# Kernel tuning notes

Measured on AMD Instinct MI355X. Metric: run time of the kernel, lower is better.

The kernel has to match this reference:

```python
import jax, jax.numpy as jnp
import numpy as np

N_HEAD, D_MODEL, D_K, D_V, POS_DIM = 8, 512, 64, 64, 2
TEMPERATURE = 8.0
LN_EPS = 1e-6


def setup_inputs() -> dict:
    key = jax.random.key(0)
    ks = jax.random.split(key, 16)
    B, S = 4, 1024
    s = 0.02
    return {
        "q": jax.random.normal(ks[0], (B, S, D_MODEL), jnp.float32),
        "k": jax.random.normal(ks[1], (B, S, D_MODEL), jnp.float32),
        "v": jax.random.normal(ks[2], (B, S, D_MODEL), jnp.float32),
        "pos_mat": jax.random.normal(ks[3], (S, S, POS_DIM), jnp.float32),
        "w_qs": jax.random.normal(ks[4], (N_HEAD * D_K, D_MODEL), jnp.float32) * s,
        "w_ks": jax.random.normal(ks[5], (N_HEAD * D_K, D_MODEL), jnp.float32) * s,
        "w_vs": jax.random.normal(ks[6], (N_HEAD * D_V, D_MODEL), jnp.float32) * s,
        "w_fc": jax.random.normal(ks[7], (D_MODEL, N_HEAD * D_V), jnp.float32) * s,
        "rp_w1": jax.random.normal(ks[8], (D_K, POS_DIM), jnp.float32) * s,
        "rp_b1": jnp.zeros((D_K,), jnp.float32),
        "rp_w2": jax.random.normal(ks[9], (D_K, D_K), jnp.float32) * s,
        "rp_b2": jnp.zeros((D_K,), jnp.float32),
        "ln_g": jnp.ones((D_MODEL,), jnp.float32),
        "ln_b": jnp.zeros((D_MODEL,), jnp.float32),
    }


def reference(q, k, v, pos_mat, w_qs, w_ks, w_vs, w_fc, rp_w1, rp_b1, rp_w2, rp_b2, ln_g, ln_b):
    B, S, _ = q.shape
    residual = q
    # projections -> (b, h, s, d)
    Q = (q @ w_qs.T).reshape(B, S, N_HEAD, D_K).transpose(0, 2, 1, 3)
    K = (k @ w_ks.T).reshape(B, S, N_HEAD, D_K).transpose(0, 2, 1, 3)
    V = (v @ w_vs.T).reshape(B, S, N_HEAD, D_V).transpose(0, 2, 1, 3)
    # relative position embedding: (s, s, d_k)
    a_k = jnp.tanh  # placeholder name avoided; compute MLP (no nonlinearity in original)
    a_k = (pos_mat @ rp_w1.T + rp_b1) @ rp_w2.T + rp_b2
    # sum over d_k of elementwise q*k*a_k, without materializing (b,h,q,k,d)
    attn = jnp.einsum("bhqd,bhkd,qkd->bhqk", Q, K, a_k) / TEMPERATURE
    attn = jax.nn.softmax(attn, axis=-1)  # dropout disabled (eval)
    out = jnp.einsum("bhqk,bhkd->bhqd", attn, V)  # (b,h,s,d_v)
    out = out.transpose(0, 2, 1, 3).reshape(B, S, N_HEAD * D_V)
    out = out @ w_fc.T + residual
    # layer norm
    mu = out.mean(-1, keepdims=True)
    var = out.var(-1, keepdims=True)
    out = (out - mu) / jnp.sqrt(var + LN_EPS) * ln_g + ln_b
    return (out, attn)
```

## Files before the change

kernel.cpp:

```cpp
#include <hip/hip_runtime.h>
#include <math.h>

#define NB   4
#define SEQ  1024
#define DMOD 512
#define NHD  8
#define DK   64

typedef unsigned short ushort_t;
typedef __attribute__((ext_vector_type(8))) short bf16x8;
typedef __attribute__((ext_vector_type(4))) float f32x4;

#define XQ_OFF   1024
#define XK_OFF   (XQ_OFF + 4194304)
#define XV_OFF   (XK_OFF + 4194304)
#define WQ_OFF   (XV_OFF + 4194304)
#define WK_OFF   (WQ_OFF + 524288)
#define WV_OFF   (WK_OFF + 524288)
#define WF_OFF   (WV_OFF + 524288)
#define QBF_OFF  (WF_OFF + 524288)
#define KBF_OFF  (QBF_OFF + 4194304)
#define VT_OFF   (KBF_OFF + 12582912)
#define O2_OFF   XQ_OFF
#define OBF_OFF  XV_OFF

__device__ inline ushort_t f2bf(float x) {
    unsigned u = __builtin_bit_cast(unsigned, x);
    unsigned r = (u + 0x7FFFu + ((u >> 16) & 1u)) >> 16;
    return (ushort_t)r;
}
__device__ inline unsigned pk2(float a, float b) {
    return (unsigned)f2bf(a) | ((unsigned)f2bf(b) << 16);
}

__global__ __launch_bounds__(64)
void prep_kernel(const float* __restrict__ rp_w1, const float* __restrict__ rp_b1,
                 const float* __restrict__ rp_w2, const float* __restrict__ rp_b2,
                 float* __restrict__ ws)
{
    int d = threadIdx.x;
    float w0 = 0.f, w1 = 0.f, cc = 0.f;
    for (int j = 0; j < 64; j++) {
        float r2 = rp_w2[d * 64 + j];
        w0 += r2 * rp_w1[j * 2 + 0];
        w1 += r2 * rp_w1[j * 2 + 1];
        cc += r2 * rp_b1[j];
    }
    ws[d] = cc + rp_b2[d];
    ws[64 + 2 * d + 0] = w0;
    ws[64 + 2 * d + 1] = w1;
}

__global__ __launch_bounds__(256)
void cvt3_kernel(const float* __restrict__ s0, const float* __restrict__ s1,
                 const float* __restrict__ s2, ushort_t* __restrict__ d0,
                 ushort_t* __restrict__ d1, ushort_t* __restrict__ d2)
{
    int t = blockIdx.x * 256 + threadIdx.x;
    const float* s = (blockIdx.y == 0) ? s0 : (blockIdx.y == 1) ? s1 : s2;
    ushort_t* d = (blockIdx.y == 0) ? d0 : (blockIdx.y == 1) ? d1 : d2;
    float4 v = *(const float4*)&s[t * 4];
    uint2 o = {pk2(v.x, v.y), pk2(v.z, v.w)};
    *(uint2*)&d[t * 4] = o;
}

__global__ __launch_bounds__(256)
void cvt4_kernel(const float* __restrict__ s0, const float* __restrict__ s1,
                 const float* __restrict__ s2, const float* __restrict__ s3,
                 ushort_t* __restrict__ d0, ushort_t* __restrict__ d1,
                 ushort_t* __restrict__ d2, ushort_t* __restrict__ d3)
{
    int t = blockIdx.x * 256 + threadIdx.x;
    const float* s = (blockIdx.y == 0) ? s0 : (blockIdx.y == 1) ? s1
                   : (blockIdx.y == 2) ? s2 : s3;
    ushort_t* d = (blockIdx.y == 0) ? d0 : (blockIdx.y == 1) ? d1
                : (blockIdx.y == 2) ? d2 : d3;
    float4 v = *(const float4*)&s[t * 4];
    uint2 o = {pk2(v.x, v.y), pk2(v.z, v.w)};
    *(uint2*)&d[t * 4] = o;
}

#define GP 72
template<int MODE>
__global__ __launch_bounds__(256)
void mfma_gemm(const ushort_t* __restrict__ X, const ushort_t* __restrict__ Wt,
               ushort_t* __restrict__ obf, float* __restrict__ ofp,
               const float* __restrict__ wc, const float* __restrict__ resid)
{
    __shared__ ushort_t Xs[64 * GP];
    __shared__ ushort_t Ws[64 * GP];
    const int n0 = blockIdx.y * 64;
    const int o0 = blockIdx.x * 64;
    const int tid = threadIdx.x;
    const int wave = tid >> 6, lane = tid & 63;
    const int m16 = lane & 15, g = lane >> 4;

    f32x4 acc[4] = {};
    for (int m0 = 0; m0 < 512; m0 += 64) {
        #pragma unroll
        for (int it = 0; it < 2; it++) {
            int idx = tid + it * 256;
            int row = idx >> 3, c8 = (idx & 7) * 8;
            *(uint4*)&Xs[row * GP + c8] = *(const uint4*)&X[(n0 + row) * 512 + m0 + c8];
            *(uint4*)&Ws[row * GP + c8] = *(const uint4*)&Wt[(o0 + row) * 512 + m0 + c8];
        }
        __syncthreads();
        #pragma unroll
        for (int kc = 0; kc < 2; kc++) {
            bf16x8 a = *(const bf16x8*)&Xs[(wave * 16 + m16) * GP + kc * 32 + g * 8];
            #pragma unroll
            for (int to = 0; to < 4; to++) {
                bf16x8 b = *(const bf16x8*)&Ws[(to * 16 + m16) * GP + kc * 32 + g * 8];
                acc[to] = __builtin_amdgcn_mfma_f32_16x16x32_bf16(a, b, acc[to], 0, 0, 0);
            }
        }
        __syncthreads();
    }
    #pragma unroll
    for (int to = 0; to < 4; to++) {
        int o = o0 + to * 16 + m16;
        #pragma unroll
        for (int r = 0; r < 4; r++) {
            int n = n0 + wave * 16 + g * 4 + r;
            float a = acc[to][r];
            int b = n >> 10, s = n & 1023, h = o >> 6, d = o & 63;
            if (MODE == 0) {
                obf[(((b * NHD + h) << 10) + s) * 64 + d] = f2bf(a);
            } else if (MODE == 1) {
                int base = ((((b * NHD + h) << 10) + s) * 192) + d;
                obf[base]       = f2bf(a * wc[d]);
                obf[base + 64]  = f2bf(a * wc[64 + 2 * d + 0]);
                obf[base + 128] = f2bf(a * wc[64 + 2 * d + 1]);
            } else if (MODE == 2) {
                obf[((b * NHD + h) * 64 + d) * 1024 + s] = f2bf(a);
            } else {
                ofp[n * 512 + o] = a + resid[n * 512 + o];
            }
        }
    }
}

#define QPITCH 72
#define KPLANE (64 * QPITCH + 8)
__global__ __launch_bounds__(256)
void score_kernel(const ushort_t* __restrict__ Qbf, const ushort_t* __restrict__ Kbf,
                  const float* __restrict__ pos, float* __restrict__ attn)
{
    __shared__ ushort_t Qs[64 * QPITCH];
    __shared__ ushort_t Ks[3 * KPLANE];
    const int bh = blockIdx.x;
    const int k0 = blockIdx.y * 64;
    const int q0 = blockIdx.z * 64;
    const int tid = threadIdx.x;

    #pragma unroll
    for (int it = 0; it < 2; it++) {
        int idx = tid + it * 256;
        int row = idx >> 3, c8 = idx & 7;
        uint4 vv = *(const uint4*)&Qbf[((bh << 10) + q0 + row) * 64 + c8 * 8];
        *(uint4*)&Qs[row * QPITCH + c8 * 8] = vv;
    }
    #pragma unroll
    for (int it = 0; it < 6; it++) {
        int idx = tid + it * 256;
        int row = idx / 24, c = idx % 24;
        int j = c >> 3, d8 = c & 7;
        uint4 vv = *(const uint4*)&Kbf[((bh << 10) + k0 + row) * 192 + c * 8];
        *(uint4*)&Ks[j * KPLANE + row * QPITCH + d8 * 8] = vv;
    }
    __syncthreads();

    const int wave = tid >> 6, lane = tid & 63;
    const int m16 = lane & 15, g = lane >> 4;

    f32x4 acc[4][3] = {};
    const ushort_t* qbase = &Qs[(wave * 16 + m16) * QPITCH + g * 8];
    #pragma unroll
    for (int kc = 0; kc < 2; kc++) {
        bf16x8 af = *(const bf16x8*)(qbase + kc * 32);
        #pragma unroll
        for (int tk = 0; tk < 4; tk++) {
            #pragma unroll
            for (int j = 0; j < 3; j++) {
                bf16x8 bfv = *(const bf16x8*)&Ks[j * KPLANE + (tk * 16 + m16) * QPITCH + kc * 32 + g * 8];
                acc[tk][j] = __builtin_amdgcn_mfma_f32_16x16x32_bf16(af, bfv, acc[tk][j], 0, 0, 0);
            }
        }
    }

    const int qrow = q0 + wave * 16 + g * 4;
    #pragma unroll
    for (int tk = 0; tk < 4; tk++) {
        int kcol = k0 + tk * 16 + m16;
        #pragma unroll
        for (int r = 0; r < 4; r++) {
            int q = qrow + r;
            float2 p = *(const float2*)&pos[(q * 1024 + kcol) * 2];
            float sc = (acc[tk][0][r] + p.x * acc[tk][1][r] + p.y * acc[tk][2][r]) * 0.125f;
            attn[((bh << 10) + q) * 1024 + kcol] = sc;
        }
    }
}

__global__ __launch_bounds__(256)
void softmax_kernel(float* __restrict__ attn)
{
    const int row = blockIdx.x;
    const int tid = threadIdx.x;
    float4 x = *(float4*)&attn[row * 1024 + tid * 4];
    float mx = fmaxf(fmaxf(x.x, x.y), fmaxf(x.z, x.w));
    for (int off = 32; off; off >>= 1) mx = fmaxf(mx, __shfl_down(mx, off, 64));
    __shared__ float red[4];
    __shared__ float bc;
    int wave = tid >> 6, lane = tid & 63;
    if (lane == 0) red[wave] = mx;
    __syncthreads();
    if (tid == 0) bc = fmaxf(fmaxf(red[0], red[1]), fmaxf(red[2], red[3]));
    __syncthreads();
    mx = bc;
    x.x = expf(x.x - mx); x.y = expf(x.y - mx);
    x.z = expf(x.z - mx); x.w = expf(x.w - mx);
    float sm = x.x + x.y + x.z + x.w;
    for (int off = 32; off; off >>= 1) sm += __shfl_down(sm, off, 64);
    __syncthreads();
    if (lane == 0) red[wave] = sm;
    __syncthreads();
    if (tid == 0) bc = red[0] + red[1] + red[2] + red[3];
    __syncthreads();
    float inv = 1.0f / bc;
    x.x *= inv; x.y *= inv; x.z *= inv; x.w *= inv;
    *(float4*)&attn[row * 1024 + tid * 4] = x;
}

__global__ __launch_bounds__(256)
void pv_mfma(const float* __restrict__ attn, const ushort_t* __restrict__ Vt,
             ushort_t* __restrict__ Obf)
{
    __shared__ ushort_t Ps[64 * GP];
    __shared__ ushort_t Vs[64 * GP];
    const int bh = blockIdx.x;
    const int q0 = blockIdx.y * 64;
    const int tid = threadIdx.x;
    const int wave = tid >> 6, lane = tid & 63;
    const int m16 = lane & 15, g = lane >> 4;

    f32x4 acc[4] = {};
    for (int k0 = 0; k0 < 1024; k0 += 64) {
        #pragma unroll
        for (int it = 0; it < 4; it++) {
            int idx = tid + it * 256;
            int row = idx >> 4, c4 = (idx & 15) * 4;
            float4 p = *(const float4*)&attn[((bh << 10) + q0 + row) * 1024 + k0 + c4];
            uint2 o = {pk2(p.x, p.y), pk2(p.z, p.w)};
            *(uint2*)&Ps[row * GP + c4] = o;
        }
        {
            int row = tid >> 2, c8 = (tid & 3) * 8;
            *(uint4*)&Vs[row * GP + c8] = *(const uint4*)&Vt[(bh * 64 + row) * 1024 + k0 + c8];
        }
        __syncthreads();
        #pragma unroll
        for (int kc = 0; kc < 2; kc++) {
            bf16x8 a = *(const bf16x8*)&Ps[(wave * 16 + m16) * GP + kc * 32 + g * 8];
            #pragma unroll
            for (int td = 0; td < 4; td++) {
                bf16x8 b = *(const bf16x8*)&Vs[(td * 16 + m16) * GP + kc * 32 + g * 8];
                acc[td] = __builtin_amdgcn_mfma_f32_16x16x32_bf16(a, b, acc[td], 0, 0, 0);
            }
        }
        __syncthreads();
    }
    const int b = bh >> 3, h = bh & 7;
    #pragma unroll
    for (int td = 0; td < 4; td++) {
        int d = td * 16 + m16;
        #pragma unroll
        for (int r = 0; r < 4; r++) {
            int q = q0 + wave * 16 + g * 4 + r;
            Obf[((b << 10) + q) * 512 + h * 64 + d] = f2bf(acc[td][r]);
        }
    }
}

__global__ __launch_bounds__(256)
void ln_kernel(const float* __restrict__ X, const float* __restrict__ g,
               const float* __restrict__ bta, float* __restrict__ out)
{
    const int row = blockIdx.x;
    const int tid = threadIdx.x;
    float2 x = *(const float2*)&X[row * 512 + tid * 2];
    float s  = x.x + x.y;
    float s2 = x.x * x.x + x.y * x.y;
    for (int off = 32; off; off >>= 1) {
        s  += __shfl_down(s, off, 64);
        s2 += __shfl_down(s2, off, 64);
    }
    __shared__ float rs[4], rs2[4];
    __shared__ float mu_s, rstd_s;
    int wave = tid >> 6, lane = tid & 63;
    if (lane == 0) { rs[wave] = s; rs2[wave] = s2; }
    __syncthreads();
    if (tid == 0) {
        float S1 = rs[0] + rs[1] + rs[2] + rs[3];
        float S2 = rs2[0] + rs2[1] + rs2[2] + rs2[3];
        float mu = S1 * (1.0f / 512.0f);
        float var = S2 * (1.0f / 512.0f) - mu * mu;
        mu_s = mu;
        rstd_s = rsqrtf(var + 1e-6f);
    }
    __syncthreads();
    float mu = mu_s, rstd = rstd_s;
    float2 gv = *(const float2*)&g[tid * 2];
    float2 bv = *(const float2*)&bta[tid * 2];
    float2 o;
    o.x = (x.x - mu) * rstd * gv.x + bv.x;
    o.y = (x.y - mu) * rstd * gv.y + bv.y;
    *(float2*)&out[row * 512 + tid * 2] = o;
}

extern "C" void kernel_launch(void* const* d_in, const int* in_sizes, int n_in,
                              void* d_out, int out_size, void* d_ws, size_t ws_size,
                              hipStream_t stream)
{
    const float* q       = (const float*)d_in[0];
    const float* k       = (const float*)d_in[1];
    const float* v       = (const float*)d_in[2];
    const float* pos_mat = (const float*)d_in[3];
    const float* w_qs    = (const float*)d_in[4];
    const float* w_ks    = (const float*)d_in[5];
    const float* w_vs    = (const float*)d_in[6];
    const float* w_fc    = (const float*)d_in[7];
    const float* rp_w1   = (const float*)d_in[8];
    const float* rp_b1   = (const float*)d_in[9];
    const float* rp_w2   = (const float*)d_in[10];
    const float* rp_b2   = (const float*)d_in[11];
    const float* ln_g    = (const float*)d_in[12];
    const float* ln_b    = (const float*)d_in[13];

    char* wsb = (char*)d_ws;
    float*    wc  = (float*)d_ws;
    ushort_t* XQ  = (ushort_t*)(wsb + XQ_OFF);
    ushort_t* XK  = (ushort_t*)(wsb + XK_OFF);
    ushort_t* XV  = (ushort_t*)(wsb + XV_OFF);
    ushort_t* WQ  = (ushort_t*)(wsb + WQ_OFF);
    ushort_t* WK  = (ushort_t*)(wsb + WK_OFF);
    ushort_t* WV  = (ushort_t*)(wsb + WV_OFF);
    ushort_t* WF  = (ushort_t*)(wsb + WF_OFF);
    ushort_t* Qbf = (ushort_t*)(wsb + QBF_OFF);
    ushort_t* Kbf = (ushort_t*)(wsb + KBF_OFF);
    ushort_t* Vt  = (ushort_t*)(wsb + VT_OFF);
    float*    O2  = (float*)(wsb + O2_OFF);
    ushort_t* Obf = (ushort_t*)(wsb + OBF_OFF);

    float* out  = (float*)d_out;
    float* attn = out + 2097152;

    prep_kernel<<<dim3(1), dim3(64), 0, stream>>>(rp_w1, rp_b1, rp_w2, rp_b2, wc);

    cvt3_kernel<<<dim3(2048, 3), 256, 0, stream>>>(q, k, v, XQ, XK, XV);
    cvt4_kernel<<<dim3(256, 4), 256, 0, stream>>>(w_qs, w_ks, w_vs, w_fc, WQ, WK, WV, WF);

    dim3 gp(8, 64);
    mfma_gemm<0><<<gp, 256, 0, stream>>>(XQ, WQ, Qbf, nullptr, nullptr, nullptr);
    mfma_gemm<1><<<gp, 256, 0, stream>>>(XK, WK, Kbf, nullptr, wc, nullptr);
    mfma_gemm<2><<<gp, 256, 0, stream>>>(XV, WV, Vt, nullptr, nullptr, nullptr);

    score_kernel<<<dim3(32, 16, 16), 256, 0, stream>>>(Qbf, Kbf, pos_mat, attn);
    softmax_kernel<<<dim3(32768), 256, 0, stream>>>(attn);
    pv_mfma<<<dim3(32, 16), 256, 0, stream>>>(attn, Vt, Obf);

    mfma_gemm<3><<<gp, 256, 0, stream>>>(Obf, WF, nullptr, O2, nullptr, q);
    ln_kernel<<<dim3(4096), 256, 0, stream>>>(O2, ln_g, ln_b, out);
}
```

Measured before the change: 345.3 us.

## Fuse score, softmax and PV into a single two-pass attention kernel

Replaces the separate score, softmax and PV kernels with one kernel per (batch-head, 64-query block). A first pass recomputes scores to build online max and sum statistics. A second pass recomputes the scores, writes normalized probabilities to attn and accumulates P·V from shared memory. This removes the fp32 attn round trips (score write, softmax read/write, PV read) in exchange for computing QK twice and reading pos twice. The grid shrinks to 512 blocks, which may reduce occupancy on a large GPU.

Result: faster. 328.0 us (-5.0%).

```diff
diff --git a/kernel.cpp b/kernel.cpp
--- a/kernel.cpp
+++ b/kernel.cpp
@@ -143,133 +143,138 @@
 #define QPITCH 72
 #define KPLANE (64 * QPITCH + 8)
 __global__ __launch_bounds__(256)
-void score_kernel(const ushort_t* __restrict__ Qbf, const ushort_t* __restrict__ Kbf,
-                  const float* __restrict__ pos, float* __restrict__ attn)
+void fused_attn(const ushort_t* __restrict__ Qbf, const ushort_t* __restrict__ Kbf,
+                const float* __restrict__ pos, const ushort_t* __restrict__ Vt,
+                float* __restrict__ attn, ushort_t* __restrict__ Obf)
 {
     __shared__ ushort_t Qs[64 * QPITCH];
     __shared__ ushort_t Ks[3 * KPLANE];
-    const int bh = blockIdx.x;
-    const int k0 = blockIdx.y * 64;
-    const int q0 = blockIdx.z * 64;
-    const int tid = threadIdx.x;
-
-    #pragma unroll
-    for (int it = 0; it < 2; it++) {
-        int idx = tid + it * 256;
-        int row = idx >> 3, c8 = idx & 7;
-        uint4 vv = *(const uint4*)&Qbf[((bh << 10) + q0 + row) * 64 + c8 * 8];
-        *(uint4*)&Qs[row * QPITCH + c8 * 8] = vv;
-    }
-    #pragma unroll
-    for (int it = 0; it < 6; it++) {
-        int idx = tid + it * 256;
-        int row = idx / 24, c = idx % 24;
-        int j = c >> 3, d8 = c & 7;
-        uint4 vv = *(const uint4*)&Kbf[((bh << 10) + k0 + row) * 192 + c * 8];
-        *(uint4*)&Ks[j * KPLANE + row * QPITCH + d8 * 8] = vv;
-    }
-    __syncthreads();
-
-    const int wave = tid >> 6, lane = tid & 63;
-    const int m16 = lane & 15, g = lane >> 4;
-
-    f32x4 acc[4][3] = {};
-    const ushort_t* qbase = &Qs[(wave * 16 + m16) * QPITCH + g * 8];
-    #pragma unroll
-    for (int kc = 0; kc < 2; kc++) {
-        bf16x8 af = *(const bf16x8*)(qbase + kc * 32);
-        #pragma unroll
-        for (int tk = 0; tk < 4; tk++) {
-            #pragma unroll
-            for (int j = 0; j < 3; j++) {
-                bf16x8 bfv = *(const bf16x8*)&Ks[j * KPLANE + (tk * 16 + m16) * QPITCH + kc * 32 + g * 8];
-                acc[tk][j] = __builtin_amdgcn_mfma_f32_16x16x32_bf16(af, bfv, acc[tk][j], 0, 0, 0);
-            }
-        }
-    }
-
-    const int qrow = q0 + wave * 16 + g * 4;
-    #pragma unroll
-    for (int tk = 0; tk < 4; tk++) {
-        int kcol = k0 + tk * 16 + m16;
-        #pragma unroll
-        for (int r = 0; r < 4; r++) {
-            int q = qrow + r;
-            float2 p = *(const float2*)&pos[(q * 1024 + kcol) * 2];
-            float sc = (acc[tk][0][r] + p.x * acc[tk][1][r] + p.y * acc[tk][2][r]) * 0.125f;
-            attn[((bh << 10) + q) * 1024 + kcol] = sc;
-        }
-    }
-}
-
-__global__ __launch_bounds__(256)
-void softmax_kernel(float* __restrict__ attn)
-{
-    const int row = blockIdx.x;
-    const int tid = threadIdx.x;
-    float4 x = *(float4*)&attn[row * 1024 + tid * 4];
-    float mx = fmaxf(fmaxf(x.x, x.y), fmaxf(x.z, x.w));
-    for (int off = 32; off; off >>= 1) mx = fmaxf(mx, __shfl_down(mx, off, 64));
-    __shared__ float red[4];
-    __shared__ float bc;
-    int wave = tid >> 6, lane = tid & 63;
-    if (lane == 0) red[wave] = mx;
-    __syncthreads();
-    if (tid == 0) bc = fmaxf(fmaxf(red[0], red[1]), fmaxf(red[2], red[3]));
-    __syncthreads();
-    mx = bc;
-    x.x = expf(x.x - mx); x.y = expf(x.y - mx);
-    x.z = expf(x.z - mx); x.w = expf(x.w - mx);
-    float sm = x.x + x.y + x.z + x.w;
-    for (int off = 32; off; off >>= 1) sm += __shfl_down(sm, off, 64);
-    __syncthreads();
-    if (lane == 0) red[wave] = sm;
-    __syncthreads();
-    if (tid == 0) bc = red[0] + red[1] + red[2] + red[3];
-    __syncthreads();
-    float inv = 1.0f / bc;
-    x.x *= inv; x.y *= inv; x.z *= inv; x.w *= inv;
-    *(float4*)&attn[row * 1024 + tid * 4] = x;
-}
-
-__global__ __launch_bounds__(256)
-void pv_mfma(const float* __restrict__ attn, const ushort_t* __restrict__ Vt,
-             ushort_t* __restrict__ Obf)
-{
-    __shared__ ushort_t Ps[64 * GP];
-    __shared__ ushort_t Vs[64 * GP];
+    __shared__ ushort_t Vs[64 * QPITCH];
+    __shared__ ushort_t Ps[64 * QPITCH];
     const int bh = blockIdx.x;
     const int q0 = blockIdx.y * 64;
     const int tid = threadIdx.x;
     const int wave = tid >> 6, lane = tid & 63;
     const int m16 = lane & 15, g = lane >> 4;
 
-    f32x4 acc[4] = {};
+    #pragma unroll
+    for (int it = 0; it < 2; it++) {
+        int idx = tid + it * 256;
+        int row = idx >> 3, c8 = (idx & 7) * 8;
+        *(uint4*)&Qs[row * QPITCH + c8] = *(const uint4*)&Qbf[((bh << 10) + q0 + row) * 64 + c8];
+    }
+    __syncthreads();
+
+    const ushort_t* qbase = &Qs[(wave * 16 + m16) * QPITCH + g * 8];
+    float m[4] = {-3.0e38f, -3.0e38f, -3.0e38f, -3.0e38f};
+    float l[4] = {0.f, 0.f, 0.f, 0.f};
+
     for (int k0 = 0; k0 < 1024; k0 += 64) {
         #pragma unroll
-        for (int it = 0; it < 4; it++) {
+        for (int it = 0; it < 6; it++) {
             int idx = tid + it * 256;
-            int row = idx >> 4, c4 = (idx & 15) * 4;
-            float4 p = *(const float4*)&attn[((bh << 10) + q0 + row) * 1024 + k0 + c4];
-            uint2 o = {pk2(p.x, p.y), pk2(p.z, p.w)};
-            *(uint2*)&Ps[row * GP + c4] = o;
-        }
-        {
-            int row = tid >> 2, c8 = (tid & 3) * 8;
-            *(uint4*)&Vs[row * GP + c8] = *(const uint4*)&Vt[(bh * 64 + row) * 1024 + k0 + c8];
-        }
-        __syncthreads();
+            int row = idx / 24, c = idx % 24;
+            int j = c >> 3, d8 = (c & 7) * 8;
+            *(uint4*)&Ks[j * KPLANE + row * QPITCH + d8] =
+                *(const uint4*)&Kbf[((bh << 10) + k0 + row) * 192 + c * 8];
+        }
+        __syncthreads();
+
+        f32x4 sc[4][3] = {};
         #pragma unroll
         for (int kc = 0; kc < 2; kc++) {
-            bf16x8 a = *(const bf16x8*)&Ps[(wave * 16 + m16) * GP + kc * 32 + g * 8];
+            bf16x8 af = *(const bf16x8*)(qbase + kc * 32);
+            #pragma unroll
+            for (int tk = 0; tk < 4; tk++)
+                #pragma unroll
+                for (int j = 0; j < 3; j++) {
+                    bf16x8 bfv = *(const bf16x8*)&Ks[j * KPLANE + (tk * 16 + m16) * QPITCH + kc * 32 + g * 8];
+                    sc[tk][j] = __builtin_amdgcn_mfma_f32_16x16x32_bf16(af, bfv, sc[tk][j], 0, 0, 0);
+                }
+        }
+
+        #pragma unroll
+        for (int r = 0; r < 4; r++) {
+            int q = q0 + wave * 16 + g * 4 + r;
+            float s4[4];
+            #pragma unroll
+            for (int tk = 0; tk < 4; tk++) {
+                float2 pp = *(const float2*)&pos[(q * 1024 + k0 + tk * 16 + m16) * 2];
+                s4[tk] = (sc[tk][0][r] + pp.x * sc[tk][1][r] + pp.y * sc[tk][2][r]) * 0.125f;
+            }
+            float tm = fmaxf(fmaxf(s4[0], s4[1]), fmaxf(s4[2], s4[3]));
+            #pragma unroll
+            for (int msk = 1; msk < 16; msk <<= 1) tm = fmaxf(tm, __shfl_xor(tm, msk, 64));
+            float nm = fmaxf(m[r], tm);
+            float ps = expf(s4[0] - nm) + expf(s4[1] - nm) + expf(s4[2] - nm) + expf(s4[3] - nm);
+            #pragma unroll
+            for (int msk = 1; msk < 16; msk <<= 1) ps += __shfl_xor(ps, msk, 64);
+            l[r] = l[r] * expf(m[r] - nm) + ps;
+            m[r] = nm;
+        }
+        __syncthreads();
+    }
+    float inv_l[4];
+    #pragma unroll
+    for (int r = 0; r < 4; r++) inv_l[r] = 1.0f / l[r];
+
+    f32x4 ao[4] = {};
+    for (int k0 = 0; k0 < 1024; k0 += 64) {
+        #pragma unroll
+        for (int it = 0; it < 6; it++) {
+            int idx = tid + it * 256;
+            int row = idx / 24, c = idx % 24;
+            int j = c >> 3, d8 = (c & 7) * 8;
+            *(uint4*)&Ks[j * KPLANE + row * QPITCH + d8] =
+                *(const uint4*)&Kbf[((bh << 10) + k0 + row) * 192 + c * 8];
+        }
+        #pragma unroll
+        for (int it = 0; it < 2; it++) {
+            int idx = tid + it * 256;
+            int row = idx >> 3, c8 = (idx & 7) * 8;
+            *(uint4*)&Vs[row * QPITCH + c8] = *(const uint4*)&Vt[(bh * 64 + row) * 1024 + k0 + c8];
+        }
+        __syncthreads();
+
+        f32x4 sc[4][3] = {};
+        #pragma unroll
+        for (int kc = 0; kc < 2; kc++) {
+            bf16x8 af = *(const bf16x8*)(qbase + kc * 32);
+            #pragma unroll
+            for (int tk = 0; tk < 4; tk++)
+                #pragma unroll
+                for (int j = 0; j < 3; j++) {
+                    bf16x8 bfv = *(const bf16x8*)&Ks[j * KPLANE + (tk * 16 + m16) * QPITCH + kc * 32 + g * 8];
+                    sc[tk][j] = __builtin_amdgcn_mfma_f32_16x16x32_bf16(af, bfv, sc[tk][j], 0, 0, 0);
+                }
+        }
+
+        #pragma unroll
+        for (int r = 0; r < 4; r++) {
+            int q = q0 + wave * 16 + g * 4 + r;
+            #pragma unroll
+            for (int tk = 0; tk < 4; tk++) {
+                float2 pp = *(const float2*)&pos[(q * 1024 + k0 + tk * 16 + m16) * 2];
+                float s = (sc[tk][0][r] + pp.x * sc[tk][1][r] + pp.y * sc[tk][2][r]) * 0.125f;
+                float p = expf(s - m[r]) * inv_l[r];
+                attn[((bh << 10) + q) * 1024 + k0 + tk * 16 + m16] = p;
+                Ps[(wave * 16 + g * 4 + r) * QPITCH + tk * 16 + m16] = f2bf(p);
+            }
+        }
+        __syncthreads();
+
+        #pragma unroll
+        for (int kc = 0; kc < 2; kc++) {
+            bf16x8 a = *(const bf16x8*)&Ps[(wave * 16 + m16) * QPITCH + kc * 32 + g * 8];
             #pragma unroll
             for (int td = 0; td < 4; td++) {
-                bf16x8 b = *(const bf16x8*)&Vs[(td * 16 + m16) * GP + kc * 32 + g * 8];
-                acc[td] = __builtin_amdgcn_mfma_f32_16x16x32_bf16(a, b, acc[td], 0, 0, 0);
-            }
-        }
-        __syncthreads();
-    }
+                bf16x8 b = *(const bf16x8*)&Vs[(td * 16 + m16) * QPITCH + kc * 32 + g * 8];
+                ao[td] = __builtin_amdgcn_mfma_f32_16x16x32_bf16(a, b, ao[td], 0, 0, 0);
+            }
+        }
+        __syncthreads();
+    }
+
     const int b = bh >> 3, h = bh & 7;
     #pragma unroll
     for (int td = 0; td < 4; td++) {
@@ -277,7 +282,7 @@
         #pragma unroll
         for (int r = 0; r < 4; r++) {
             int q = q0 + wave * 16 + g * 4 + r;
-            Obf[((b << 10) + q) * 512 + h * 64 + d] = f2bf(acc[td][r]);
+            Obf[((b << 10) + q) * 512 + h * 64 + d] = f2bf(ao[td][r]);
         }
     }
 }
@@ -365,9 +370,7 @@
     mfma_gemm<1><<<gp, 256, 0, stream>>>(XK, WK, Kbf, nullptr, wc, nullptr);
     mfma_gemm<2><<<gp, 256, 0, stream>>>(XV, WV, Vt, nullptr, nullptr, nullptr);
 
-    score_kernel<<<dim3(32, 16, 16), 256, 0, stream>>>(Qbf, Kbf, pos_mat, attn);
-    softmax_kernel<<<dim3(32768), 256, 0, stream>>>(attn);
-    pv_mfma<<<dim3(32, 16), 256, 0, stream>>>(attn, Vt, Obf);
+    fused_attn<<<dim3(32, 16), 256, 0, stream>>>(Qbf, Kbf, pos_mat, Vt, attn, Obf);
 
     mfma_gemm<3><<<gp, 256, 0, stream>>>(Obf, WF, nullptr, O2, nullptr, q);
     ln_kernel<<<dim3(4096), 256, 0, stream>>>(O2, ln_g, ln_b, out);
```
